# Kernel tuning notes

Hardware: AMD Instinct MI355X
Metric: run time of the kernel (lower is better)

## Reference

```python
import jax, jax.numpy as jnp
import numpy as np

E = 64          # moe_num_experts
H = 1024        # hidden_size
F = 2816        # per_expert_ff_dim
T = 4096        # total tokens (equal split: 64 per expert)


def setup_inputs() -> dict:
    key = jax.random.key(0)
    k1, k2, k3, k4 = jax.random.split(key, 4)
    s = 1.0 / np.sqrt(H)
    return {
        "x": jax.random.normal(k1, (T, H), dtype=jnp.float32),
        "tokens_per_expert": jnp.full((E,), T // E, dtype=jnp.int32),
        "w1": jax.random.normal(k2, (E * F, H), dtype=jnp.float32) * s,
        "w3": jax.random.normal(k3, (E * F, H), dtype=jnp.float32) * s,
        "w2": jax.random.normal(k4, (E * F, H), dtype=jnp.float32) * s,
    }


def reference(x, tokens_per_expert, w1, w3, w2):
    # Tokens are grouped contiguously per expert with an equal split,
    # so the variable-size grouped GEMM (gg.ops.gmm) reduces to a batched einsum.
    tpe = x.shape[0] // E
    xg = x.reshape(E, tpe, H)            # [E, t, h]
    w1e = w1.reshape(E, F, H)
    w3e = w3.reshape(E, F, H)
    w2e = w2.reshape(E, F, H)
    # gmm(x, w1, trans_b=True): per-expert x @ w1[e].T
    h1 = jnp.einsum("eth,efh->etf", xg, w1e)   # [E, t, f]
    h3 = jnp.einsum("eth,efh->etf", xg, w3e)   # [E, t, f]
    gated = jax.nn.silu(h1) * h3               # SwiGLU
    # gmm(gated, w2): per-expert gated @ w2[e]  ([t,f] @ [f,h])
    out = jnp.einsum("etf,efh->eth", gated, w2e)
    return out.reshape(-1, H)
```

## Files before the change

### kernel.cpp

```cpp
#include <hip/hip_runtime.h>
#include <hip/hip_bf16.h>

#define NE   64
#define NH   1024
#define NF   2816
#define TPE  64
#define PITCH 72

typedef __attribute__((ext_vector_type(8))) short bf16x8;
typedef __attribute__((ext_vector_type(4))) float f32x4;

__device__ __forceinline__ ushort f2bf(float f) {
    union { float f; unsigned u; } v; v.f = f;
    unsigned r = v.u + 0x7fffu + ((v.u >> 16) & 1u);
    return (ushort)(r >> 16);
}

__device__ __forceinline__ bf16x8 cvt8(f32x4 lo, f32x4 hi) {
    bf16x8 r;
    #pragma unroll
    for (int j = 0; j < 4; ++j) {
        r[j]     = (short)f2bf(lo[j]);
        r[4 + j] = (short)f2bf(hi[j]);
    }
    return r;
}

__global__ __launch_bounds__(256)
void xcast(const float* __restrict__ x, ushort* __restrict__ xb) {
    const int i = blockIdx.x * 256 + threadIdx.x;
    const f32x4 a = *(const f32x4*)(x + (size_t)i * 8);
    const f32x4 b = *(const f32x4*)(x + (size_t)i * 8 + 4);
    *(bf16x8*)(xb + (size_t)i * 8) = cvt8(a, b);
}

__global__ __launch_bounds__(256, 2)
void k1_gate(const ushort* __restrict__ xb,
             const float* __restrict__ w1,
             const float* __restrict__ w3,
             ushort* __restrict__ g) {
    __shared__ ushort lW1[64 * PITCH];
    __shared__ ushort lW3[64 * PITCH];

    const int jt   = blockIdx.x;
    const int e    = blockIdx.y;
    const int tid  = threadIdx.x;
    const int lane = tid & 63;
    const int wid  = tid >> 6;
    const int m15  = lane & 15;
    const int hi   = lane >> 4;
    const int mrow = wid * 16 + m15;

    const ushort* xA = xb + (size_t)e * TPE * NH + (size_t)mrow * NH;
    const float*  B1 = w1 + ((size_t)e * NF + (size_t)jt * 64) * NH;
    const float*  B3 = w3 + ((size_t)e * NF + (size_t)jt * 64) * NH;

    f32x4 acc1[4], acc3[4];
    #pragma unroll
    for (int nf = 0; nf < 4; ++nf) {
        acc1[nf] = f32x4{0.f, 0.f, 0.f, 0.f};
        acc3[nf] = f32x4{0.f, 0.f, 0.f, 0.f};
    }

    const int srow = tid >> 4;
    const int sc4  = (tid & 15) * 4;

    for (int kt = 0; kt < NH / 64; ++kt) {
        const size_t kb = (size_t)kt * 64;
        __syncthreads();
        #pragma unroll
        for (int r = 0; r < 4; ++r) {
            const int row = srow + r * 16;
            const size_t goff = (size_t)row * NH + kb + sc4;
            const float4 v1 = *(const float4*)(B1 + goff);
            const float4 v3 = *(const float4*)(B3 + goff);
            ushort4 u1, u3;
            u1.x = f2bf(v1.x); u1.y = f2bf(v1.y); u1.z = f2bf(v1.z); u1.w = f2bf(v1.w);
            u3.x = f2bf(v3.x); u3.y = f2bf(v3.y); u3.z = f2bf(v3.z); u3.w = f2bf(v3.w);
            *(ushort4*)(&lW1[row * PITCH + sc4]) = u1;
            *(ushort4*)(&lW3[row * PITCH + sc4]) = u3;
        }
        __syncthreads();

        #pragma unroll
        for (int ks = 0; ks < 2; ++ks) {
            const int koff = ks * 32 + hi * 8;
            const bf16x8 af = *(const bf16x8*)(xA + kb + koff);
            #pragma unroll
            for (int nf = 0; nf < 4; ++nf) {
                const int bo = (nf * 16 + m15) * PITCH + koff;
                const bf16x8 b1 = *(const bf16x8*)(&lW1[bo]);
                acc1[nf] = __builtin_amdgcn_mfma_f32_16x16x32_bf16(af, b1, acc1[nf], 0, 0, 0);
                const bf16x8 b3 = *(const bf16x8*)(&lW3[bo]);
                acc3[nf] = __builtin_amdgcn_mfma_f32_16x16x32_bf16(af, b3, acc3[nf], 0, 0, 0);
            }
        }
    }

    #pragma unroll
    for (int nf = 0; nf < 4; ++nf) {
        #pragma unroll
        for (int i = 0; i < 4; ++i) {
            const float h1v = acc1[nf][i];
            const float h3v = acc3[nf][i];
            const float s   = (h1v / (1.f + __expf(-h1v))) * h3v;
            const int row = wid * 16 + (hi * 4) + i;
            const int col = jt * 64 + nf * 16 + m15;
            const size_t t = (size_t)e * TPE + row;
            g[t * NF + col] = f2bf(s);
        }
    }
}

__global__ __launch_bounds__(256, 2)
void k2_down(const ushort* __restrict__ g,
             const float* __restrict__ w2,
             float* __restrict__ out) {
    __shared__ ushort lA[64 * PITCH];
    __shared__ ushort lB[64 * PITCH];

    const int jt   = blockIdx.x;
    const int e    = blockIdx.y;
    const int tid  = threadIdx.x;
    const int lane = tid & 63;
    const int wid  = tid >> 6;

    const ushort* A = g  + (size_t)e * TPE * NF;
    const float*  B = w2 + (size_t)e * NF * NH + (size_t)jt * 64;
    float* O = out + (size_t)e * TPE * NH + (size_t)jt * 64;

    f32x4 acc[4];
    for (int nf = 0; nf < 4; ++nf) acc[nf] = f32x4{0.f, 0.f, 0.f, 0.f};

    for (int kt = 0; kt < NF / 64; ++kt) {
        __syncthreads();
        #pragma unroll
        for (int r = 0; r < 2; ++r) {
            const int q   = tid + r * 256;
            const int row = q >> 3;
            const int k8  = (q & 7) * 8;
            *(bf16x8*)(&lA[row * PITCH + k8]) =
                *(const bf16x8*)(A + (size_t)row * NF + kt * 64 + k8);
        }
        {
            const int n  = tid & 63;
            const int kq = (tid >> 6) * 4;
            #pragma unroll
            for (int r = 0; r < 4; ++r) {
                const int ks = kq + r * 16;
                const size_t base = (size_t)(kt * 64 + ks) * NH + n;
                const float f0 = B[base];
                const float f1 = B[base + NH];
                const float f2 = B[base + 2 * (size_t)NH];
                const float f3 = B[base + 3 * (size_t)NH];
                ushort4 b;
                b.x = f2bf(f0); b.y = f2bf(f1); b.z = f2bf(f2); b.w = f2bf(f3);
                *(ushort4*)(&lB[n * PITCH + ks]) = b;
            }
        }
        __syncthreads();

        const int mrow = wid * 16 + (lane & 15);
        #pragma unroll
        for (int ks = 0; ks < 2; ++ks) {
            const int koff = ks * 32 + ((lane >> 4) * 8);
            const bf16x8 af = *(const bf16x8*)(&lA[mrow * PITCH + koff]);
            #pragma unroll
            for (int nf = 0; nf < 4; ++nf) {
                const bf16x8 bfr = *(const bf16x8*)(&lB[(nf * 16 + (lane & 15)) * PITCH + koff]);
                acc[nf] = __builtin_amdgcn_mfma_f32_16x16x32_bf16(af, bfr, acc[nf], 0, 0, 0);
            }
        }
    }

    #pragma unroll
    for (int nf = 0; nf < 4; ++nf) {
        #pragma unroll
        for (int i = 0; i < 4; ++i) {
            const int row = wid * 16 + ((lane >> 4) * 4) + i;
            const int col = nf * 16 + (lane & 15);
            O[(size_t)row * NH + col] = acc[nf][i];
        }
    }
}

extern "C" void kernel_launch(void* const* d_in, const int* in_sizes, int n_in,
                              void* d_out, int out_size, void* d_ws, size_t ws_size,
                              hipStream_t stream) {
    const float* x  = (const float*)d_in[0];
    const float* w1 = (const float*)d_in[2];
    const float* w3 = (const float*)d_in[3];
    const float* w2 = (const float*)d_in[4];
    float* out = (float*)d_out;
    ushort* gated = (ushort*)d_ws;
    ushort* xbf   = (ushort*)((char*)d_ws + (32u << 20));

    xcast<<<dim3((TPE * NE * NH) / (256 * 8)), dim3(256), 0, stream>>>(x, xbf);

    dim3 g1(NF / 64, NE);
    k1_gate<<<g1, dim3(256), 0, stream>>>(xbf, w1, w3, gated);

    dim3 g2(NH / 64, NE);
    k2_down<<<g2, dim3(256), 0, stream>>>(gated, w2, out);
}
```

Before: 518.4 us.

## Shrink gate kernel tile to 16 columns with full-K weight staging in LDS

The gate/up kernel now processes 16 F-columns per block instead of 64, staging the entire K=1024 slice of w1 and w3 into LDS once with a single barrier rather than looping over 16 K-tiles with two barriers each. This quadruples the grid, giving more blocks to hide the HBM-bound fp32 weight streaming, and removes the per-tile synchronisation. In exchange each block re-reads all of x per 16 columns (four times more x traffic, mostly cache hits), uses about 66 KB of LDS per block, which may limit occupancy, and does fewer MFMAs per block.

```diff
diff --git a/kernel.cpp b/kernel.cpp
--- a/kernel.cpp
+++ b/kernel.cpp
@@ -5,7 +5,8 @@
 #define NH   1024
 #define NF   2816
 #define TPE  64
-#define PITCH 72
+#define PITCH  72
+#define WPITCH 1032
 
 typedef __attribute__((ext_vector_type(8))) short bf16x8;
 typedef __attribute__((ext_vector_type(4))) float f32x4;
@@ -39,8 +40,8 @@
              const float* __restrict__ w1,
              const float* __restrict__ w3,
              ushort* __restrict__ g) {
-    __shared__ ushort lW1[64 * PITCH];
-    __shared__ ushort lW3[64 * PITCH];
+    __shared__ ushort lW1[16 * WPITCH];
+    __shared__ ushort lW3[16 * WPITCH];
 
     const int jt   = blockIdx.x;
     const int e    = blockIdx.y;
@@ -51,64 +52,46 @@
     const int hi   = lane >> 4;
     const int mrow = wid * 16 + m15;
 
-    const ushort* xA = xb + (size_t)e * TPE * NH + (size_t)mrow * NH;
-    const float*  B1 = w1 + ((size_t)e * NF + (size_t)jt * 64) * NH;
-    const float*  B3 = w3 + ((size_t)e * NF + (size_t)jt * 64) * NH;
+    const float* B1 = w1 + ((size_t)e * NF + (size_t)jt * 16) * NH;
+    const float* B3 = w3 + ((size_t)e * NF + (size_t)jt * 16) * NH;
 
-    f32x4 acc1[4], acc3[4];
     #pragma unroll
-    for (int nf = 0; nf < 4; ++nf) {
-        acc1[nf] = f32x4{0.f, 0.f, 0.f, 0.f};
-        acc3[nf] = f32x4{0.f, 0.f, 0.f, 0.f};
+    for (int r = 0; r < 8; ++r) {
+        const int p    = r * 256 + tid;
+        const int row  = p >> 7;
+        const int colp = p & 127;
+        const size_t goff = (size_t)row * NH + (size_t)colp * 8;
+        const f32x4 a1 = *(const f32x4*)(B1 + goff);
+        const f32x4 b1 = *(const f32x4*)(B1 + goff + 4);
+        const f32x4 a3 = *(const f32x4*)(B3 + goff);
+        const f32x4 b3 = *(const f32x4*)(B3 + goff + 4);
+        *(bf16x8*)(&lW1[row * WPITCH + colp * 8]) = cvt8(a1, b1);
+        *(bf16x8*)(&lW3[row * WPITCH + colp * 8]) = cvt8(a3, b3);
     }
+    __syncthreads();
 
-    const int srow = tid >> 4;
-    const int sc4  = (tid & 15) * 4;
+    f32x4 acc1 = f32x4{0.f, 0.f, 0.f, 0.f};
+    f32x4 acc3 = f32x4{0.f, 0.f, 0.f, 0.f};
+    const ushort* xrow = xb + ((size_t)e * TPE + mrow) * NH;
 
-    for (int kt = 0; kt < NH / 64; ++kt) {
-        const size_t kb = (size_t)kt * 64;
-        __syncthreads();
-        #pragma unroll
-        for (int r = 0; r < 4; ++r) {
-            const int row = srow + r * 16;
-            const size_t goff = (size_t)row * NH + kb + sc4;
-            const float4 v1 = *(const float4*)(B1 + goff);
-            const float4 v3 = *(const float4*)(B3 + goff);
-            ushort4 u1, u3;
-            u1.x = f2bf(v1.x); u1.y = f2bf(v1.y); u1.z = f2bf(v1.z); u1.w = f2bf(v1.w);
-            u3.x = f2bf(v3.x); u3.y = f2bf(v3.y); u3.z = f2bf(v3.z); u3.w = f2bf(v3.w);
-            *(ushort4*)(&lW1[row * PITCH + sc4]) = u1;
-            *(ushort4*)(&lW3[row * PITCH + sc4]) = u3;
-        }
-        __syncthreads();
-
-        #pragma unroll
-        for (int ks = 0; ks < 2; ++ks) {
-            const int koff = ks * 32 + hi * 8;
-            const bf16x8 af = *(const bf16x8*)(xA + kb + koff);
-            #pragma unroll
-            for (int nf = 0; nf < 4; ++nf) {
-                const int bo = (nf * 16 + m15) * PITCH + koff;
-                const bf16x8 b1 = *(const bf16x8*)(&lW1[bo]);
-                acc1[nf] = __builtin_amdgcn_mfma_f32_16x16x32_bf16(af, b1, acc1[nf], 0, 0, 0);
-                const bf16x8 b3 = *(const bf16x8*)(&lW3[bo]);
-                acc3[nf] = __builtin_amdgcn_mfma_f32_16x16x32_bf16(af, b3, acc3[nf], 0, 0, 0);
-            }
-        }
+    #pragma unroll 8
+    for (int kk = 0; kk < 32; ++kk) {
+        const int ko = kk * 32 + hi * 8;
+        const bf16x8 af = *(const bf16x8*)(xrow + ko);
+        const bf16x8 b1 = *(const bf16x8*)(&lW1[m15 * WPITCH + ko]);
+        acc1 = __builtin_amdgcn_mfma_f32_16x16x32_bf16(af, b1, acc1, 0, 0, 0);
+        const bf16x8 b3 = *(const bf16x8*)(&lW3[m15 * WPITCH + ko]);
+        acc3 = __builtin_amdgcn_mfma_f32_16x16x32_bf16(af, b3, acc3, 0, 0, 0);
     }
 
     #pragma unroll
-    for (int nf = 0; nf < 4; ++nf) {
-        #pragma unroll
-        for (int i = 0; i < 4; ++i) {
-            const float h1v = acc1[nf][i];
-            const float h3v = acc3[nf][i];
-            const float s   = (h1v / (1.f + __expf(-h1v))) * h3v;
-            const int row = wid * 16 + (hi * 4) + i;
-            const int col = jt * 64 + nf * 16 + m15;
-            const size_t t = (size_t)e * TPE + row;
-            g[t * NF + col] = f2bf(s);
-        }
+    for (int i = 0; i < 4; ++i) {
+        const float h1v = acc1[i];
+        const float h3v = acc3[i];
+        const float s   = (h1v / (1.f + __expf(-h1v))) * h3v;
+        const int row = wid * 16 + hi * 4 + i;
+        const int col = jt * 16 + m15;
+        g[((size_t)e * TPE + row) * NF + col] = f2bf(s);
     }
 }
 
@@ -197,7 +180,7 @@
 
     xcast<<<dim3((TPE * NE * NH) / (256 * 8)), dim3(256), 0, stream>>>(x, xbf);
 
-    dim3 g1(NF / 64, NE);
+    dim3 g1(NF / 16, NE);
     k1_gate<<<g1, dim3(256), 0, stream>>>(xbf, w1, w3, gated);
 
     dim3 g2(NH / 64, NE);
```

Result: slower. 553.2 us (+6.7%).

## Split fused gate GEMM into separate w1 and w3 passes via bf16 intermediate

Applied to the files above, without the earlier changes.

Splits the fused gate kernel, which computed both w1 and w3 projections per block, into two launches of a templated single-weight GEMM. The first launch writes h1 to workspace as bf16, and the second computes the w3 projection and applies SwiGLU using the stored h1. This halves LDS use and accumulator registers per block, which may raise occupancy. In exchange it adds a launch, an extra write and read of the h1 intermediate, re-reads x a second time, and rounds h1 to bf16 before the SiLU.

```diff
diff --git a/kernel.cpp b/kernel.cpp
--- a/kernel.cpp
+++ b/kernel.cpp
@@ -14,6 +14,11 @@
     union { float f; unsigned u; } v; v.f = f;
     unsigned r = v.u + 0x7fffu + ((v.u >> 16) & 1u);
     return (ushort)(r >> 16);
+}
+
+__device__ __forceinline__ float bf2f(ushort u) {
+    union { unsigned u; float f; } v; v.u = ((unsigned)u) << 16;
+    return v.f;
 }
 
 __device__ __forceinline__ bf16x8 cvt8(f32x4 lo, f32x4 hi) {
@@ -34,13 +39,13 @@
     *(bf16x8*)(xb + (size_t)i * 8) = cvt8(a, b);
 }
 
+template <int GATE>
 __global__ __launch_bounds__(256, 2)
-void k1_gate(const ushort* __restrict__ xb,
-             const float* __restrict__ w1,
-             const float* __restrict__ w3,
-             ushort* __restrict__ g) {
-    __shared__ ushort lW1[64 * PITCH];
-    __shared__ ushort lW3[64 * PITCH];
+void k1_mm(const ushort* __restrict__ xb,
+           const float* __restrict__ w,
+           const ushort* __restrict__ h1in,
+           ushort* __restrict__ outp) {
+    __shared__ ushort lW[64 * PITCH];
 
     const int jt   = blockIdx.x;
     const int e    = blockIdx.y;
@@ -51,16 +56,12 @@
     const int hi   = lane >> 4;
     const int mrow = wid * 16 + m15;
 
-    const ushort* xA = xb + (size_t)e * TPE * NH + (size_t)mrow * NH;
-    const float*  B1 = w1 + ((size_t)e * NF + (size_t)jt * 64) * NH;
-    const float*  B3 = w3 + ((size_t)e * NF + (size_t)jt * 64) * NH;
-
-    f32x4 acc1[4], acc3[4];
-    #pragma unroll
-    for (int nf = 0; nf < 4; ++nf) {
-        acc1[nf] = f32x4{0.f, 0.f, 0.f, 0.f};
-        acc3[nf] = f32x4{0.f, 0.f, 0.f, 0.f};
-    }
+    const ushort* xA = xb + ((size_t)e * TPE + mrow) * NH;
+    const float*  B  = w  + ((size_t)e * NF + (size_t)jt * 64) * NH;
+
+    f32x4 acc[4];
+    #pragma unroll
+    for (int nf = 0; nf < 4; ++nf) acc[nf] = f32x4{0.f, 0.f, 0.f, 0.f};
 
     const int srow = tid >> 4;
     const int sc4  = (tid & 15) * 4;
@@ -71,14 +72,10 @@
         #pragma unroll
         for (int r = 0; r < 4; ++r) {
             const int row = srow + r * 16;
-            const size_t goff = (size_t)row * NH + kb + sc4;
-            const float4 v1 = *(const float4*)(B1 + goff);
-            const float4 v3 = *(const float4*)(B3 + goff);
-            ushort4 u1, u3;
-            u1.x = f2bf(v1.x); u1.y = f2bf(v1.y); u1.z = f2bf(v1.z); u1.w = f2bf(v1.w);
-            u3.x = f2bf(v3.x); u3.y = f2bf(v3.y); u3.z = f2bf(v3.z); u3.w = f2bf(v3.w);
-            *(ushort4*)(&lW1[row * PITCH + sc4]) = u1;
-            *(ushort4*)(&lW3[row * PITCH + sc4]) = u3;
+            const float4 v = *(const float4*)(B + (size_t)row * NH + kb + sc4);
+            ushort4 u;
+            u.x = f2bf(v.x); u.y = f2bf(v.y); u.z = f2bf(v.z); u.w = f2bf(v.w);
+            *(ushort4*)(&lW[row * PITCH + sc4]) = u;
         }
         __syncthreads();
 
@@ -88,11 +85,8 @@
             const bf16x8 af = *(const bf16x8*)(xA + kb + koff);
             #pragma unroll
             for (int nf = 0; nf < 4; ++nf) {
-                const int bo = (nf * 16 + m15) * PITCH + koff;
-                const bf16x8 b1 = *(const bf16x8*)(&lW1[bo]);
-                acc1[nf] = __builtin_amdgcn_mfma_f32_16x16x32_bf16(af, b1, acc1[nf], 0, 0, 0);
-                const bf16x8 b3 = *(const bf16x8*)(&lW3[bo]);
-                acc3[nf] = __builtin_amdgcn_mfma_f32_16x16x32_bf16(af, b3, acc3[nf], 0, 0, 0);
+                const bf16x8 bw = *(const bf16x8*)(&lW[(nf * 16 + m15) * PITCH + koff]);
+                acc[nf] = __builtin_amdgcn_mfma_f32_16x16x32_bf16(af, bw, acc[nf], 0, 0, 0);
             }
         }
     }
@@ -101,13 +95,17 @@
     for (int nf = 0; nf < 4; ++nf) {
         #pragma unroll
         for (int i = 0; i < 4; ++i) {
-            const float h1v = acc1[nf][i];
-            const float h3v = acc3[nf][i];
-            const float s   = (h1v / (1.f + __expf(-h1v))) * h3v;
-            const int row = wid * 16 + (hi * 4) + i;
+            const int row = wid * 16 + hi * 4 + i;
             const int col = jt * 64 + nf * 16 + m15;
-            const size_t t = (size_t)e * TPE + row;
-            g[t * NF + col] = f2bf(s);
+            const size_t idx = ((size_t)e * TPE + row) * NF + col;
+            if (GATE) {
+                const float h1v = bf2f(h1in[idx]);
+                const float h3v = acc[nf][i];
+                const float s   = (h1v / (1.f + __expf(-h1v))) * h3v;
+                outp[idx] = f2bf(s);
+            } else {
+                outp[idx] = f2bf(acc[nf][i]);
+            }
         }
     }
 }
@@ -194,11 +192,13 @@
     float* out = (float*)d_out;
     ushort* gated = (ushort*)d_ws;
     ushort* xbf   = (ushort*)((char*)d_ws + (32u << 20));
+    ushort* h1    = (ushort*)((char*)d_ws + (48u << 20));
 
     xcast<<<dim3((TPE * NE * NH) / (256 * 8)), dim3(256), 0, stream>>>(x, xbf);
 
     dim3 g1(NF / 64, NE);
-    k1_gate<<<g1, dim3(256), 0, stream>>>(xbf, w1, w3, gated);
+    k1_mm<0><<<g1, dim3(256), 0, stream>>>(xbf, w1, nullptr, h1);
+    k1_mm<1><<<g1, dim3(256), 0, stream>>>(xbf, w3, h1, gated);
 
     dim3 g2(NH / 64, NE);
     k2_down<<<g2, dim3(256), 0, stream>>>(gated, w2, out);
```

Result: faster. 504.6 us (-2.7%).
